# Kernel optimization log

Measured on AMD Instinct MI355X. Metric: run time of the kernel, lower is better.

Reference implementation:

```python
import jax, jax.numpy as jnp
import numpy as np

D_MODEL = 1024
D_STATE = 16
D_CONV = 4
EXPAND = 2
D_INNER = EXPAND * D_MODEL          # 2048
DT_RANK = D_INNER // 16             # 128
BATCH = 2
SEQLEN = 1024


def _silu(x):
    return x * jax.nn.sigmoid(x)


def setup_inputs() -> dict:
    key = jax.random.key(0)
    ks = jax.random.split(key, 8)
    s = 0.02
    A_init = jnp.tile(jnp.arange(1, D_STATE + 1, dtype=jnp.float32)[None, :], (D_INNER, 1))
    return {
        "x": jax.random.normal(ks[0], (BATCH, SEQLEN, D_MODEL), jnp.float32),
        "W_in": jax.random.normal(ks[1], (D_MODEL, 2 * D_INNER), jnp.float32) * s,
        "conv_k": jax.random.normal(ks[2], (D_CONV, 1, D_INNER), jnp.float32) * s,  # (kw, in/groups, out)
        "conv_b": jnp.zeros((D_INNER,), jnp.float32),
        "W_xproj": jax.random.normal(ks[3], (D_INNER, DT_RANK + 2 * D_STATE), jnp.float32) * s,
        "W_dt": jax.random.normal(ks[4], (DT_RANK, D_INNER), jnp.float32) * s,
        "b_dt": jnp.zeros((D_INNER,), jnp.float32),
        "A_log": jnp.log(A_init),
        "D": jnp.ones((D_INNER,), jnp.float32),
        "W_out": jax.random.normal(ks[5], (D_INNER, D_MODEL), jnp.float32) * s,
    }


def reference(x, W_in, conv_k, conv_b, W_xproj, W_dt, b_dt, A_log, D, W_out):
    # in_proj and gate split
    xz = x @ W_in                                   # (B, L, 2*Di)
    x_in, z = jnp.split(xz, 2, axis=-1)             # each (B, L, Di)

    # depthwise causal conv1d: left-pad by d_conv-1 (keras padding='causal')
    xp = jnp.pad(x_in, ((0, 0), (D_CONV - 1, 0), (0, 0)))
    x_in = jax.lax.conv_general_dilated(
        xp, conv_k, window_strides=(1,), padding='VALID',
        dimension_numbers=('NWC', 'WIO', 'NWC'),
        feature_group_count=D_INNER) + conv_b
    u = _silu(x_in)                                 # (B, L, Di)

    # input-dependent SSM params
    x_dbl = u @ W_xproj                             # (B, L, dt_rank + 2*N)
    dt_low, Bm, Cm = jnp.split(x_dbl, [DT_RANK, DT_RANK + D_STATE], axis=-1)
    dt = jax.nn.softplus(dt_low @ W_dt + b_dt)      # (B, L, Di)
    A = -jnp.exp(A_log)                             # (Di, N)
    dA = jnp.exp(jnp.einsum('bld,dn->bldn', dt, A)) # (B, L, Di, N)
    dB = jnp.einsum('bld,bln->bldn', dt, Bm)        # (B, L, Di, N)

    # selective scan over sequence length
    def step(h, e):
        a_t, b_t, u_t, c_t = e                      # (B,Di,N), (B,Di,N), (B,Di), (B,N)
        h = a_t * h + b_t * u_t[..., None]
        y_t = jnp.einsum('bdn,bn->bd', h, c_t)
        return h, y_t

    h0 = jnp.zeros((x.shape[0], D_INNER, D_STATE), dtype=x.dtype)
    xs = (jnp.swapaxes(dA, 0, 1), jnp.swapaxes(dB, 0, 1),
          jnp.swapaxes(u, 0, 1), jnp.swapaxes(Cm, 0, 1))
    _, yT = jax.lax.scan(step, h0, xs)              # (L, B, Di)
    y = jnp.swapaxes(yT, 0, 1) + u * D              # skip connection

    return (y * _silu(z)) @ W_out                   # (B, L, d_model)
```

## Files before the change

### kernel.cpp

```cpp
#include <hip/hip_runtime.h>
#include <hip/hip_bf16.h>

#define D_MODEL 1024
#define D_STATE 16
#define D_CONV 4
#define D_INNER 2048
#define DT_RANK 128
#define BATCH 2
#define SEQLEN 1024
#define XCOLS 160
#define NCHUNK 32
#define LCHUNK 32

typedef __hip_bfloat16 bf16;
typedef __attribute__((ext_vector_type(8))) short short8;
typedef __attribute__((ext_vector_type(4))) float f32x4;

__device__ __forceinline__ unsigned short f2bf_bits(float f) {
    bf16 h = __float2bfloat16(f);
    return *(unsigned short*)&h;
}

__device__ __forceinline__ float bfbits2f(short s) {
    union { float f; unsigned u; } v;
    v.u = ((unsigned)(unsigned short)s) << 16;
    return v.f;
}

__device__ __forceinline__ float softplus_f(float x) {
    return fmaxf(x, 0.f) + __logf(1.f + __expf(-fabsf(x)));
}

__device__ __forceinline__ float silu_f(float x) {
    return x / (1.f + __expf(-x));
}

__device__ __forceinline__ void load16_lds(void* lds, const void* g) {
    __builtin_amdgcn_global_load_lds(
        (const __attribute__((address_space(1))) unsigned int*)g,
        (__attribute__((address_space(3))) unsigned int*)lds, 16, 0, 0);
}

__device__ __forceinline__ void transpose_tile(const float* __restrict__ B,
                                               bf16* __restrict__ Bt,
                                               int K, int N, int nt, int kt,
                                               float (*t)[33], int tid)
{
    const int tx = tid & 31, ty = tid >> 5;
    const int n0 = nt * 32, k0 = kt * 32;
    #pragma unroll
    for (int r = 0; r < 4; ++r) {
        int n = n0 + tx;
        t[ty + r * 8][tx] = (n < N) ? B[(size_t)(k0 + ty + r * 8) * N + n] : 0.f;
    }
    __syncthreads();
    #pragma unroll
    for (int r = 0; r < 4; ++r)
        Bt[(size_t)(n0 + ty + r * 8) * K + k0 + tx] = __float2bfloat16(t[tx][ty + r * 8]);
}

__global__ __launch_bounds__(256)
void prep_kernel(const float* __restrict__ x, bf16* __restrict__ x_bf,
                 const float* __restrict__ W_in, bf16* __restrict__ Win_t,
                 const float* __restrict__ W_xproj, bf16* __restrict__ Wxp_t,
                 const float* __restrict__ W_dt, bf16* __restrict__ Wdt_t,
                 const float* __restrict__ W_out, bf16* __restrict__ Wout_t,
                 const float* __restrict__ A_log, float* __restrict__ Aneg)
{
    __shared__ float t[32][33];
    const int tid = threadIdx.x;
    int blk = blockIdx.x;
    if (blk < 4096) {
        transpose_tile(W_in, Win_t, D_MODEL, 2 * D_INNER, blk & 127, blk >> 7, t, tid);
        return;
    }
    blk -= 4096;
    if (blk < 512) {
        transpose_tile(W_xproj, Wxp_t, D_INNER, XCOLS, blk & 7, blk >> 3, t, tid);
        return;
    }
    blk -= 512;
    if (blk < 256) {
        transpose_tile(W_dt, Wdt_t, DT_RANK, D_INNER, blk & 63, blk >> 6, t, tid);
        return;
    }
    blk -= 256;
    if (blk < 2048) {
        transpose_tile(W_out, Wout_t, D_INNER, D_MODEL, blk & 31, blk >> 5, t, tid);
        return;
    }
    blk -= 2048;
    if (blk < 2048) {
        int i = blk * 256 + tid;
        float4 v = ((const float4*)x)[i];
        ushort4 p;
        p.x = f2bf_bits(v.x); p.y = f2bf_bits(v.y);
        p.z = f2bf_bits(v.z); p.w = f2bf_bits(v.w);
        ((ushort4*)x_bf)[i] = p;
        return;
    }
    blk -= 2048;
    {
        int i = blk * 256 + tid;
        Aneg[i] = -__expf(A_log[i]);
    }
}

template<int BN, int EPI>
__global__ __launch_bounds__(256)
void gemm_mfma(const bf16* __restrict__ A, const bf16* __restrict__ Bt,
               float* __restrict__ C, bf16* __restrict__ Cb,
               bf16* __restrict__ Cb2,
               const float* __restrict__ bias,
               int M, int N, int K, int ldc, int kchunk)
{
    constexpr int WN = (BN == 128) ? 64 : 32;
    constexpr int NJ = WN / 16;
    __shared__ short As[2][128 * 32];
    __shared__ short Bs[2][BN * 32];
    const int tid = threadIdx.x;
    const int lane = tid & 63, wave = tid >> 6;
    const int wm = (wave >> 1) * 64, wn = (wave & 1) * WN;

    const int gx = gridDim.x, gy = gridDim.y;
    const int total = gx * gy * gridDim.z;
    const int hwid = (blockIdx.z * gy + blockIdx.y) * gx + blockIdx.x;
    const int nid = (hwid & 7) * (total >> 3) + (hwid >> 3);
    const int bz = nid / (gx * gy);
    const int rem = nid - bz * (gx * gy);
    const int bx = rem / gy;
    const int by = rem - bx * gy;

    const int row0 = by * 128, col0 = bx * BN;
    const int r_m = lane & 15, r_q = lane >> 4;
    const int kstart = bz * kchunk;
    float* Cz = C + (size_t)bz * M * ldc;

    const int srow = tid >> 2;
    const int schk = ((tid & 3) ^ ((srow >> 1) & 3)) * 8;
    const bf16* Ag0 = A  + (size_t)(row0 + srow)      * K + kstart + schk;
    const bf16* Ag1 = A  + (size_t)(row0 + srow + 64) * K + kstart + schk;
    const bf16* Bg0 = Bt + (size_t)(col0 + srow)      * K + kstart + schk;
    const bf16* Bg1 = Bt + (size_t)(col0 + srow + 64) * K + kstart + schk;

    const int cx = (r_q ^ ((r_m >> 1) & 3)) * 8;

    f32x4 acc[4][NJ];
    #pragma unroll
    for (int i = 0; i < 4; ++i)
        #pragma unroll
        for (int j = 0; j < NJ; ++j)
            #pragma unroll
            for (int r = 0; r < 4; ++r) acc[i][j][r] = 0.f;

#define GEMM_STAGE(BUF, KOFF)                                                   \
    {                                                                           \
        load16_lds(&As[BUF][8 * tid], Ag0 + (KOFF));                            \
        load16_lds(&As[BUF][8 * tid + 2048], Ag1 + (KOFF));                     \
        load16_lds(&Bs[BUF][8 * tid], Bg0 + (KOFF));                            \
        if (BN == 128) load16_lds(&Bs[BUF][8 * tid + 2048], Bg1 + (KOFF));      \
    }

#define GEMM_COMPUTE(BUF)                                                       \
    {                                                                           \
        short8 af[4], bfr[NJ];                                                  \
        _Pragma("unroll")                                                       \
        for (int i = 0; i < 4; ++i)                                             \
            af[i] = *(const short8*)&As[BUF][(wm + i * 16 + r_m) * 32 + cx];    \
        _Pragma("unroll")                                                       \
        for (int j = 0; j < NJ; ++j)                                            \
            bfr[j] = *(const short8*)&Bs[BUF][(wn + j * 16 + r_m) * 32 + cx];   \
        _Pragma("unroll")                                                       \
        for (int i = 0; i < 4; ++i)                                             \
            _Pragma("unroll")                                                   \
            for (int j = 0; j < NJ; ++j)                                        \
                acc[i][j] = __builtin_amdgcn_mfma_f32_16x16x32_bf16(            \
                    af[i], bfr[j], acc[i][j], 0, 0, 0);                         \
    }

    GEMM_STAGE(0, 0);
    __syncthreads();
    for (int k0 = 0; k0 < kchunk; k0 += 64) {
        GEMM_STAGE(1, k0 + 32);
        GEMM_COMPUTE(0);
        __syncthreads();
        if (k0 + 64 < kchunk) GEMM_STAGE(0, k0 + 64);
        GEMM_COMPUTE(1);
        __syncthreads();
    }
#undef GEMM_STAGE
#undef GEMM_COMPUTE

    #pragma unroll
    for (int i = 0; i < 4; ++i) {
        #pragma unroll
        for (int j = 0; j < NJ; ++j) {
            int row = row0 + wm + i * 16 + r_q * 4;
            int col = col0 + wn + j * 16 + r_m;
            if (col < N) {
                if (EPI == 1) {
                    float bv = bias[col];
                    #pragma unroll
                    for (int r = 0; r < 4; ++r)
                        Cb[(size_t)(row + r) * ldc + col] =
                            __float2bfloat16(softplus_f(acc[i][j][r] + bv));
                } else if (EPI == 2) {
                    if (col < 2048) {
                        #pragma unroll
                        for (int r = 0; r < 4; ++r)
                            Cb2[(size_t)(row + r) * ldc + col] =
                                __float2bfloat16(acc[i][j][r]);
                    } else {
                        int zc = col - 2048;
                        #pragma unroll
                        for (int r = 0; r < 4; ++r)
                            Cb[(size_t)(row + r) * ldc + zc] =
                                __float2bfloat16(silu_f(acc[i][j][r]));
                    }
                } else {
                    #pragma unroll
                    for (int r = 0; r < 4; ++r)
                        Cz[(size_t)(row + r) * ldc + col] = acc[i][j][r];
                }
            }
        }
    }
}

__global__ __launch_bounds__(256)
void reduce_xdbl(const float* __restrict__ Cpart, float* __restrict__ x_dbl,
                 bf16* __restrict__ dtA_bf)
{
    int i4 = blockIdx.x * 256 + threadIdx.x;
    if (i4 >= 2048 * (XCOLS / 4)) return;
    int r = i4 / (XCOLS / 4), c4 = i4 - r * (XCOLS / 4);
    float4 s = {0.f, 0.f, 0.f, 0.f};
    #pragma unroll
    for (int z = 0; z < 8; ++z) {
        float4 v = *(const float4*)&Cpart[(size_t)z * 2048 * 256 + (size_t)r * 256 + c4 * 4];
        s.x += v.x; s.y += v.y; s.z += v.z; s.w += v.w;
    }
    *(float4*)&x_dbl[(size_t)r * XCOLS + c4 * 4] = s;
    if (c4 < DT_RANK / 4) {
        ushort4 p;
        p.x = f2bf_bits(s.x); p.y = f2bf_bits(s.y);
        p.z = f2bf_bits(s.z); p.w = f2bf_bits(s.w);
        *(ushort4*)&dtA_bf[(size_t)r * DT_RANK + c4 * 4] = p;
    }
}

__global__ __launch_bounds__(256)
void reduce_out(const float* __restrict__ Cpart, float* __restrict__ out)
{
    int i = blockIdx.x * 256 + threadIdx.x;
    const float4* p0 = (const float4*)Cpart;
    const float4* p1 = p0 + (size_t)2048 * 1024 / 4;
    float4 a = p0[i], b = p1[i];
    float4 r; r.x = a.x + b.x; r.y = a.y + b.y; r.z = a.z + b.z; r.w = a.w + b.w;
    ((float4*)out)[i] = r;
}

__global__ __launch_bounds__(256)
void conv_silu_kernel(const bf16* __restrict__ xd,
                      const float* __restrict__ conv_k,
                      const float* __restrict__ conv_b,
                      bf16* __restrict__ u_bf)
{
    int idx8 = blockIdx.x * 256 + threadIdx.x;
    int d8 = idx8 & (D_INNER / 8 - 1);
    int t = (idx8 >> 8) & (SEQLEN - 1);
    int b = idx8 >> 18;
    float acc[8];
    {
        float4 b0 = ((const float4*)conv_b)[d8 * 2];
        float4 b1 = ((const float4*)conv_b)[d8 * 2 + 1];
        acc[0] = b0.x; acc[1] = b0.y; acc[2] = b0.z; acc[3] = b0.w;
        acc[4] = b1.x; acc[5] = b1.y; acc[6] = b1.z; acc[7] = b1.w;
    }
    #pragma unroll
    for (int k = 0; k < D_CONV; ++k) {
        int tt = t + k - (D_CONV - 1);
        if (tt >= 0) {
            short8 xv = ((const short8*)xd)[(size_t)(b * SEQLEN + tt) * (D_INNER / 8) + d8];
            float4 k0 = ((const float4*)conv_k)[k * (D_INNER / 4) + d8 * 2];
            float4 k1 = ((const float4*)conv_k)[k * (D_INNER / 4) + d8 * 2 + 1];
            acc[0] = fmaf(bfbits2f(xv[0]), k0.x, acc[0]);
            acc[1] = fmaf(bfbits2f(xv[1]), k0.y, acc[1]);
            acc[2] = fmaf(bfbits2f(xv[2]), k0.z, acc[2]);
            acc[3] = fmaf(bfbits2f(xv[3]), k0.w, acc[3]);
            acc[4] = fmaf(bfbits2f(xv[4]), k1.x, acc[4]);
            acc[5] = fmaf(bfbits2f(xv[5]), k1.y, acc[5]);
            acc[6] = fmaf(bfbits2f(xv[6]), k1.z, acc[6]);
            acc[7] = fmaf(bfbits2f(xv[7]), k1.w, acc[7]);
        }
    }
    short8 r;
    #pragma unroll
    for (int j = 0; j < 8; ++j)
        r[j] = (short)f2bf_bits(acc[j] / (1.f + __expf(-acc[j])));
    ((short8*)u_bf)[idx8] = r;
}

__global__ __launch_bounds__(256)
void scan_phase1(const bf16* __restrict__ dt_sb,
                 const float* __restrict__ Aneg,
                 const bf16* __restrict__ u_bf,
                 const float* __restrict__ x_dbl,
                 float* __restrict__ Pst, float* __restrict__ Sst)
{
    __shared__ float Bsm[LCHUNK][16];
    const int d = blockIdx.x * 256 + threadIdx.x;
    const int c = blockIdx.y, b = blockIdx.z;
    const int t0 = c * LCHUNK;
    for (int i = threadIdx.x; i < LCHUNK * 16; i += 256) {
        int tt = i >> 4, n = i & 15;
        Bsm[tt][n] = x_dbl[(size_t)(b * SEQLEN + t0 + tt) * XCOLS + DT_RANK + n];
    }
    float A_row[D_STATE];
    const float4* a4 = (const float4*)(Aneg + d * D_STATE);
    #pragma unroll
    for (int q = 0; q < 4; ++q) {
        float4 v = a4[q];
        A_row[q*4+0] = v.x; A_row[q*4+1] = v.y; A_row[q*4+2] = v.z; A_row[q*4+3] = v.w;
    }
    __syncthreads();
    float P[D_STATE], S[D_STATE];
    #pragma unroll
    for (int n = 0; n < D_STATE; ++n) { P[n] = 1.f; S[n] = 0.f; }
    const bf16* dpp = dt_sb + (size_t)(b * SEQLEN + t0) * D_INNER + d;
    const bf16* upp = u_bf + (size_t)(b * SEQLEN + t0) * D_INNER + d;
    #pragma unroll 4
    for (int t = 0; t < LCHUNK; ++t) {
        float dtv = __bfloat162float(dpp[(size_t)t * D_INNER]);
        float du = dtv * __bfloat162float(upp[(size_t)t * D_INNER]);
        const float4* b4 = (const float4*)&Bsm[t][0];
        #pragma unroll
        for (int q = 0; q < 4; ++q) {
            float4 v = b4[q];
            float Bn[4] = {v.x, v.y, v.z, v.w};
            #pragma unroll
            for (int e = 0; e < 4; ++e) {
                int n = q * 4 + e;
                float a = __expf(dtv * A_row[n]);
                P[n] *= a;
                S[n] = fmaf(a, S[n], du * Bn[e]);
            }
        }
    }
    const size_t base = ((size_t)(b * NCHUNK + c) * D_STATE) * D_INNER + d;
    #pragma unroll
    for (int n = 0; n < D_STATE; ++n) {
        Pst[base + (size_t)n * D_INNER] = P[n];
        Sst[base + (size_t)n * D_INNER] = S[n];
    }
}

__global__ __launch_bounds__(256)
void scan_phase2(const float* __restrict__ Pst, float* __restrict__ Sst)
{
    const int d = blockIdx.x * 256 + threadIdx.x;
    const int n = blockIdx.y;
    const int b = blockIdx.z;
    float Pv[NCHUNK], Sv[NCHUNK];
    #pragma unroll
    for (int c = 0; c < NCHUNK; ++c) {
        const size_t idx = ((size_t)(b * NCHUNK + c) * D_STATE + n) * D_INNER + d;
        Pv[c] = Pst[idx];
        Sv[c] = Sst[idx];
    }
    float h = 0.f;
    #pragma unroll
    for (int c = 0; c < NCHUNK; ++c) {
        float hin = h;
        h = fmaf(Pv[c], h, Sv[c]);
        Sv[c] = hin;
    }
    #pragma unroll
    for (int c = 0; c < NCHUNK; ++c) {
        const size_t idx = ((size_t)(b * NCHUNK + c) * D_STATE + n) * D_INNER + d;
        Sst[idx] = Sv[c];
    }
}

__global__ __launch_bounds__(256)
void scan_phase3(const bf16* __restrict__ dt_sb,
                 const float* __restrict__ Aneg,
                 const bf16* __restrict__ u_bf,
                 const float* __restrict__ x_dbl,
                 const float* __restrict__ Dvec,
                 const bf16* __restrict__ sz_bf,
                 const float* __restrict__ hin,
                 bf16* __restrict__ g_bf)
{
    __shared__ float BCs[LCHUNK][32];
    const int d = blockIdx.x * 256 + threadIdx.x;
    const int c = blockIdx.y, b = blockIdx.z;
    const int t0 = c * LCHUNK;
    for (int i = threadIdx.x; i < LCHUNK * 32; i += 256) {
        int tt = i >> 5, col = i & 31;
        BCs[tt][col] = x_dbl[(size_t)(b * SEQLEN + t0 + tt) * XCOLS + DT_RANK + col];
    }
    float A_row[D_STATE];
    const float4* a4 = (const float4*)(Aneg + d * D_STATE);
    #pragma unroll
    for (int q = 0; q < 4; ++q) {
        float4 v = a4[q];
        A_row[q*4+0] = v.x; A_row[q*4+1] = v.y; A_row[q*4+2] = v.z; A_row[q*4+3] = v.w;
    }
    const float Dd = Dvec[d];
    __syncthreads();
    float h[D_STATE];
    const size_t base = ((size_t)(b * NCHUNK + c) * D_STATE) * D_INNER + d;
    #pragma unroll
    for (int n = 0; n < D_STATE; ++n) h[n] = hin[base + (size_t)n * D_INNER];
    const bf16* dpp = dt_sb + (size_t)(b * SEQLEN + t0) * D_INNER + d;
    const bf16* upp = u_bf + (size_t)(b * SEQLEN + t0) * D_INNER + d;
    const bf16* zpp = sz_bf + (size_t)(b * SEQLEN + t0) * D_INNER + d;
    bf16* gpp = g_bf + (size_t)(b * SEQLEN + t0) * D_INNER + d;
    #pragma unroll 4
    for (int t = 0; t < LCHUNK; ++t) {
        float dtv = __bfloat162float(dpp[(size_t)t * D_INNER]);
        float uv = __bfloat162float(upp[(size_t)t * D_INNER]);
        float sz = __bfloat162float(zpp[(size_t)t * D_INNER]);
        float du = dtv * uv;
        float y = 0.f;
        const float4* bc4 = (const float4*)&BCs[t][0];
        #pragma unroll
        for (int q = 0; q < 4; ++q) {
            float4 v = bc4[q];
            float4 w = bc4[q + 4];
            float Bn[4] = {v.x, v.y, v.z, v.w};
            float Cn[4] = {w.x, w.y, w.z, w.w};
            #pragma unroll
            for (int e = 0; e < 4; ++e) {
                int n = q * 4 + e;
                float a = __expf(dtv * A_row[n]);
                h[n] = fmaf(a, h[n], du * Bn[e]);
                y = fmaf(h[n], Cn[e], y);
            }
        }
        float gy = y + uv * Dd;
        gpp[(size_t)t * D_INNER] = __float2bfloat16(gy * sz);
    }
}

extern "C" void kernel_launch(void* const* d_in, const int* in_sizes, int n_in,
                              void* d_out, int out_size, void* d_ws, size_t ws_size,
                              hipStream_t stream)
{
    const float* x      = (const float*)d_in[0];
    const float* W_in   = (const float*)d_in[1];
    const float* conv_k = (const float*)d_in[2];
    const float* conv_b = (const float*)d_in[3];
    const float* W_xproj= (const float*)d_in[4];
    const float* W_dt   = (const float*)d_in[5];
    const float* b_dt   = (const float*)d_in[6];
    const float* A_log  = (const float*)d_in[7];
    const float* Dvec   = (const float*)d_in[8];
    const float* W_out  = (const float*)d_in[9];
    float* out = (float*)d_out;

    const int BL = BATCH * SEQLEN;

    float* ws     = (float*)d_ws;
    float* x_dbl  = ws;
    float* Pst    = x_dbl + (size_t)BL * XCOLS;
    float* Sst    = Pst + (size_t)BATCH * NCHUNK * D_STATE * D_INNER;
    float* Aneg   = Sst + (size_t)BATCH * NCHUNK * D_STATE * D_INNER;
    float* Cpart  = Aneg + 32768;
    bf16*  x_bf   = (bf16*)Cpart;
    bf16* Win_t  = (bf16*)(Cpart + (size_t)4 * 1048576);
    bf16* xd_bf  = Win_t + (size_t)4096 * 1024;
    bf16* u_bf   = xd_bf + (size_t)BL * D_INNER;
    bf16* sz_bf  = u_bf  + (size_t)BL * D_INNER;
    bf16* Wxp_t  = sz_bf + (size_t)BL * D_INNER;
    bf16* dtA_bf = Wxp_t + (size_t)256 * 2048;
    bf16* Wdt_t  = dtA_bf+ (size_t)BL * DT_RANK;
    bf16* g_bf   = Wdt_t + (size_t)2048 * 128;
    bf16* Wout_t = g_bf  + (size_t)BL * D_INNER;
    bf16* dt_sb  = Wout_t+ (size_t)1024 * 2048;

    prep_kernel<<<4096 + 512 + 256 + 2048 + 2048 + 128, 256, 0, stream>>>(
        x, x_bf, W_in, Win_t, W_xproj, Wxp_t, W_dt, Wdt_t, W_out, Wout_t, A_log, Aneg);

    gemm_mfma<64, 2><<<dim3(64, 16, 1), 256, 0, stream>>>(
        x_bf, Win_t, nullptr, sz_bf, xd_bf, nullptr, BL, 2 * D_INNER, D_MODEL, D_INNER, D_MODEL);

    conv_silu_kernel<<<(BL * D_INNER / 8) / 256, 256, 0, stream>>>(xd_bf, conv_k, conv_b, u_bf);

    gemm_mfma<64, 0><<<dim3(3, 16, 8), 256, 0, stream>>>(
        u_bf, Wxp_t, Cpart, nullptr, nullptr, nullptr, BL, 256, D_INNER, 256, 256);
    reduce_xdbl<<<(BL * (XCOLS / 4) + 255) / 256, 256, 0, stream>>>(Cpart, x_dbl, dtA_bf);

    gemm_mfma<64, 1><<<dim3(32, 16, 1), 256, 0, stream>>>(
        dtA_bf, Wdt_t, nullptr, dt_sb, nullptr, b_dt, BL, D_INNER, DT_RANK, D_INNER, DT_RANK);

    scan_phase1<<<dim3(D_INNER / 256, NCHUNK, BATCH), 256, 0, stream>>>(
        dt_sb, Aneg, u_bf, x_dbl, Pst, Sst);
    scan_phase2<<<dim3(D_INNER / 256, D_STATE, BATCH), 256, 0, stream>>>(Pst, Sst);
    scan_phase3<<<dim3(D_INNER / 256, NCHUNK, BATCH), 256, 0, stream>>>(
        dt_sb, Aneg, u_bf, x_dbl, Dvec, sz_bf, Sst, g_bf);

    gemm_mfma<64, 0><<<dim3(16, 16, 2), 256, 0, stream>>>(
        g_bf, Wout_t, Cpart, nullptr, nullptr, nullptr, BL, D_MODEL, D_INNER, D_MODEL, D_INNER / 2);
    reduce_out<<<(BL * D_MODEL / 4) / 256, 256, 0, stream>>>(Cpart, out);
}
```

Baseline: 229.5 us.

## Deepen GEMM K-tile to 64 and widen in_proj N-tile to 128

The shared MFMA GEMM now stages 64-wide K slices instead of 32. It uses a new 8-way XOR swizzle and issues two MFMA k-steps per buffer, which halves the number of barriers and stage iterations per K. The in_proj GEMM also switches from a 64-wide to a 128-wide N tile with half the grid, so each A-tile load is reused across more output columns. The cost is a larger LDS footprint, up to 64 KB per block for BN=128, which can lower occupancy and latency hiding.

```diff
diff --git a/kernel.cpp b/kernel.cpp
--- a/kernel.cpp
+++ b/kernel.cpp
@@ -116,8 +116,9 @@
 {
     constexpr int WN = (BN == 128) ? 64 : 32;
     constexpr int NJ = WN / 16;
-    __shared__ short As[2][128 * 32];
-    __shared__ short Bs[2][BN * 32];
+    constexpr int BL_ = BN / 32;
+    __shared__ short As[2][128 * 64];
+    __shared__ short Bs[2][BN * 64];
     const int tid = threadIdx.x;
     const int lane = tid & 63, wave = tid >> 6;
     const int wm = (wave >> 1) * 64, wn = (wave & 1) * WN;
@@ -136,14 +137,10 @@
     const int kstart = bz * kchunk;
     float* Cz = C + (size_t)bz * M * ldc;
 
-    const int srow = tid >> 2;
-    const int schk = ((tid & 3) ^ ((srow >> 1) & 3)) * 8;
-    const bf16* Ag0 = A  + (size_t)(row0 + srow)      * K + kstart + schk;
-    const bf16* Ag1 = A  + (size_t)(row0 + srow + 64) * K + kstart + schk;
-    const bf16* Bg0 = Bt + (size_t)(col0 + srow)      * K + kstart + schk;
-    const bf16* Bg1 = Bt + (size_t)(col0 + srow + 64) * K + kstart + schk;
-
-    const int cx = (r_q ^ ((r_m >> 1) & 3)) * 8;
+    const int srow = tid >> 3;
+    const int schk = ((tid & 7) ^ (srow & 7)) * 8;
+    const bf16* Ag = A  + (size_t)(row0 + srow) * K + kstart + schk;
+    const bf16* Bg = Bt + (size_t)(col0 + srow) * K + kstart + schk;
 
     f32x4 acc[4][NJ];
     #pragma unroll
@@ -155,36 +152,46 @@
 
 #define GEMM_STAGE(BUF, KOFF)                                                   \
     {                                                                           \
-        load16_lds(&As[BUF][8 * tid], Ag0 + (KOFF));                            \
-        load16_lds(&As[BUF][8 * tid + 2048], Ag1 + (KOFF));                     \
-        load16_lds(&Bs[BUF][8 * tid], Bg0 + (KOFF));                            \
-        if (BN == 128) load16_lds(&Bs[BUF][8 * tid + 2048], Bg1 + (KOFF));      \
+        _Pragma("unroll")                                                       \
+        for (int L = 0; L < 4; ++L)                                             \
+            load16_lds(&As[BUF][2048 * L + 8 * tid],                            \
+                       Ag + (size_t)(L * 32) * K + (KOFF));                     \
+        _Pragma("unroll")                                                       \
+        for (int L = 0; L < BL_; ++L)                                           \
+            load16_lds(&Bs[BUF][2048 * L + 8 * tid],                            \
+                       Bg + (size_t)(L * 32) * K + (KOFF));                     \
     }
 
 #define GEMM_COMPUTE(BUF)                                                       \
     {                                                                           \
-        short8 af[4], bfr[NJ];                                                  \
+        short8 af[2][4], bfr[2][NJ];                                            \
         _Pragma("unroll")                                                       \
-        for (int i = 0; i < 4; ++i)                                             \
-            af[i] = *(const short8*)&As[BUF][(wm + i * 16 + r_m) * 32 + cx];    \
-        _Pragma("unroll")                                                       \
-        for (int j = 0; j < NJ; ++j)                                            \
-            bfr[j] = *(const short8*)&Bs[BUF][(wn + j * 16 + r_m) * 32 + cx];   \
-        _Pragma("unroll")                                                       \
-        for (int i = 0; i < 4; ++i)                                             \
+        for (int kk = 0; kk < 2; ++kk) {                                        \
+            const int cxk = ((kk * 4 + r_q) ^ (r_m & 7)) * 8;                   \
+            _Pragma("unroll")                                                   \
+            for (int i = 0; i < 4; ++i)                                         \
+                af[kk][i] = *(const short8*)&As[BUF][(wm + i * 16 + r_m) * 64 + cxk]; \
             _Pragma("unroll")                                                   \
             for (int j = 0; j < NJ; ++j)                                        \
-                acc[i][j] = __builtin_amdgcn_mfma_f32_16x16x32_bf16(            \
-                    af[i], bfr[j], acc[i][j], 0, 0, 0);                         \
+                bfr[kk][j] = *(const short8*)&Bs[BUF][(wn + j * 16 + r_m) * 64 + cxk]; \
+        }                                                                       \
+        _Pragma("unroll")                                                       \
+        for (int kk = 0; kk < 2; ++kk)                                          \
+            _Pragma("unroll")                                                   \
+            for (int i = 0; i < 4; ++i)                                         \
+                _Pragma("unroll")                                               \
+                for (int j = 0; j < NJ; ++j)                                    \
+                    acc[i][j] = __builtin_amdgcn_mfma_f32_16x16x32_bf16(        \
+                        af[kk][i], bfr[kk][j], acc[i][j], 0, 0, 0);             \
     }
 
     GEMM_STAGE(0, 0);
     __syncthreads();
-    for (int k0 = 0; k0 < kchunk; k0 += 64) {
-        GEMM_STAGE(1, k0 + 32);
+    for (int k0 = 0; k0 < kchunk; k0 += 128) {
+        GEMM_STAGE(1, k0 + 64);
         GEMM_COMPUTE(0);
         __syncthreads();
-        if (k0 + 64 < kchunk) GEMM_STAGE(0, k0 + 64);
+        if (k0 + 128 < kchunk) GEMM_STAGE(0, k0 + 128);
         GEMM_COMPUTE(1);
         __syncthreads();
     }
@@ -483,7 +490,7 @@
     prep_kernel<<<4096 + 512 + 256 + 2048 + 2048 + 128, 256, 0, stream>>>(
         x, x_bf, W_in, Win_t, W_xproj, Wxp_t, W_dt, Wdt_t, W_out, Wout_t, A_log, Aneg);
 
-    gemm_mfma<64, 2><<<dim3(64, 16, 1), 256, 0, stream>>>(
+    gemm_mfma<128, 2><<<dim3(32, 16, 1), 256, 0, stream>>>(
         x_bf, Win_t, nullptr, sz_bf, xd_bf, nullptr, BL, 2 * D_INNER, D_MODEL, D_INNER, D_MODEL);
 
     conv_silu_kernel<<<(BL * D_INNER / 8) / 256, 256, 0, stream>>>(xd_bf, conv_k, conv_b, u_bf);
```

New measurement: 225.1 us. About the same (-1.9%).
